# Optimization experiments

Measured on AMD Instinct MI355X. Metric: run time of the kernel, lower is better.

Reference implementation:

```python
import jax, jax.numpy as jnp
import numpy as np

T_MAX = 0.3  # clamp ceiling for effective opacity (t_max init kwarg)


def setup_inputs() -> dict:
    key = jax.random.key(0)
    k0, k1, k2 = jax.random.split(key, 3)
    B, n_blobs, d_s, d_f = 1024, 131072, 64, 256
    return {
        "query": jax.random.normal(k0, (B, d_s), dtype=jnp.float32),
        "mu": jax.random.normal(k1, (n_blobs, d_s), dtype=jnp.float32) * 0.02,
        "log_var": jnp.zeros((n_blobs, d_s), dtype=jnp.float32),
        "raw_alpha": jnp.zeros((n_blobs,), dtype=jnp.float32),
        "features": jax.random.normal(k2, (n_blobs, d_f), dtype=jnp.float32) * 0.02,
        "log_tau": jnp.asarray(np.log(128.0), dtype=jnp.float32),
        "k": 16,
    }


def reference(query, mu, log_var, raw_alpha, features, log_tau, k):
    # query: [B, d_s]; mu/log_var: [N, d_s]; features: [N, d_f]
    tau = jnp.exp(log_tau)
    inv_var = jnp.exp(-log_var)                              # [N, d_s]
    # Mahalanobis distance expanded to avoid the [B, N, d_s] diff tensor:
    # sum_d (q - mu)^2 * iv = q^2.iv - 2 q.(mu*iv) + sum(mu^2*iv)
    q2 = jnp.einsum('bd,nd->bn', query * query, inv_var)      # [B, N]
    cross = jnp.einsum('bd,nd->bn', query, mu * inv_var)      # [B, N]
    m2 = jnp.sum(mu * mu * inv_var, axis=-1)                  # [N]
    mahal = q2 - 2.0 * cross + m2[None, :]
    K_all = jnp.exp(-0.5 * mahal / tau)                       # [B, N]
    alpha = jax.nn.sigmoid(raw_alpha)                         # [N]
    scores = K_all * alpha[None, :]
    top_scores, top_idx = jax.lax.top_k(scores, k)            # [B, k]

    # Gather selected blobs and recompute exact kernel (as in the original render)
    blob_feats = features[top_idx]                            # [B, k, d_f]
    blob_mu = mu[top_idx]                                     # [B, k, d_s]
    blob_iv = jnp.exp(-log_var[top_idx])                      # [B, k, d_s]
    diff = query[:, None, :] - blob_mu                        # [B, k, d_s]
    mahal_k = jnp.sum(diff * diff * blob_iv, axis=-1)         # [B, k]
    K_topk = jnp.exp(-0.5 * mahal_k / tau)
    blob_alpha = alpha[top_idx]                               # [B, k]

    # Alpha compositing in log space
    eff = jnp.minimum(blob_alpha * K_topk, T_MAX / k)         # [B, k]
    log_1m = jnp.log1p(-jnp.minimum(eff, 1.0 - 1e-6))
    log_cum = jnp.cumsum(log_1m, axis=-1)
    log_T = jnp.concatenate(
        [jnp.zeros_like(log_cum[:, :1]), log_cum[:, :-1]], axis=-1)
    weights = eff * jnp.exp(log_T)                            # [B, k]
    blob_meaning = jnp.einsum('bk,bkd->bd', weights, blob_feats)  # [B, d_f]
    t_residual = jnp.exp(log_cum[:, -1])                      # [B]
    return blob_meaning, t_residual
```

## Files before the change

kernel.cpp:

```cpp
#include <hip/hip_runtime.h>
#include <math.h>

#define BQ    1024
#define NB    131072
#define DS    64
#define DF    256
#define KSEL  16

#define QT    128
#define BC    64
#define PCH   64
#define NCHUNK (NB / BC)
#define CHUNKS_PER_BLK (NCHUNK/PCH)

#define CH_BYTES   32768
#define SPLIT_OFF  16384

typedef __bf16 bf16x8 __attribute__((ext_vector_type(8)));
typedef float  f32x4  __attribute__((ext_vector_type(4)));
typedef unsigned long long u64;

#define ENC_NEGINF 0x007FFFFFu

__device__ __forceinline__ unsigned map_f32(float s) {
    unsigned u = __float_as_uint(s);
    return (u & 0x80000000u) ? ~u : (u | 0x80000000u);
}

__device__ __forceinline__ float unmap_f32(unsigned e) {
    return __uint_as_float((e & 0x80000000u) ? (e & 0x7FFFFFFFu) : ~e);
}

__device__ __forceinline__ void async_cp16(const void* g, void* l) {
    __builtin_amdgcn_global_load_lds(
        (const __attribute__((address_space(1))) unsigned int*)g,
        (__attribute__((address_space(3))) unsigned int*)l, 16, 0, 0);
}

__global__ __launch_bounds__(256)
void prep_kernel(const float* __restrict__ mu,
                 const float* __restrict__ log_var,
                 const float* __restrict__ raw_alpha,
                 const float* __restrict__ log_tau_p,
                 char* __restrict__ bprep,
                 float* __restrict__ m2a,
                 unsigned* __restrict__ gcut)
{
    int gid  = blockIdx.x * 256 + threadIdx.x;
    if (gid < BQ) gcut[gid] = ENC_NEGINF;
    int blob = gid >> 3;
    int dd   = gid & 7;

    const float* mrow = mu      + (size_t)blob * DS + dd * 8;
    const float* vrow = log_var + (size_t)blob * DS + dd * 8;
    float4 ma = ((const float4*)mrow)[0], mb = ((const float4*)mrow)[1];
    float4 va = ((const float4*)vrow)[0], vb = ((const float4*)vrow)[1];
    float m[8] = {ma.x, ma.y, ma.z, ma.w, mb.x, mb.y, mb.z, mb.w};
    float lv[8] = {va.x, va.y, va.z, va.w, vb.x, vb.y, vb.z, vb.w};

    bf16x8 hiv, liv, hmv, lmv;
    float p = 0.0f;
    #pragma unroll
    for (int j = 0; j < 8; ++j) {
        float iv = __expf(-lv[j]);
        float mv = m[j] * iv;
        p += m[j] * mv;
        __bf16 h1 = (__bf16)iv;  hiv[j] = h1; liv[j] = (__bf16)(iv - (float)h1);
        __bf16 h2 = (__bf16)mv;  hmv[j] = h2; lmv[j] = (__bf16)(mv - (float)h2);
    }
    p += __shfl_xor(p, 1);
    p += __shfl_xor(p, 2);
    p += __shfl_xor(p, 4);

    int c  = blob >> 6;
    int nt = (blob >> 4) & 3;
    int bl = blob & 15;
    int lane  = (dd & 3) * 16 + bl;
    int ks_iv = dd >> 2;
    int ks_mv = 2 + (dd >> 2);
    size_t b_iv = (size_t)c * CH_BYTES + nt * 4096 + ks_iv * 1024 + lane * 16;
    size_t b_mv = (size_t)c * CH_BYTES + nt * 4096 + ks_mv * 1024 + lane * 16;
    *(bf16x8*)(bprep + b_iv)             = hiv;
    *(bf16x8*)(bprep + b_iv + SPLIT_OFF) = liv;
    *(bf16x8*)(bprep + b_mv)             = hmv;
    *(bf16x8*)(bprep + b_mv + SPLIT_OFF) = lmv;

    if (dd == 0) {
        float la = -log1pf(__expf(-raw_alpha[blob]));
        float inv_nhit = -2.0f * __expf(log_tau_p[0]);
        m2a[blob] = p + la * inv_nhit;
    }
}

__device__ __forceinline__ void ins16(float (&ts)[16], int (&ti)[16],
                                      float& mymin, float s, int idx)
{
    float v0[8]; int j0[8];
    #pragma unroll
    for (int i = 0; i < 8; ++i) {
        bool b = ts[2*i+1] < ts[2*i];
        v0[i] = b ? ts[2*i+1] : ts[2*i];
        j0[i] = (i << 1) | (b ? 1 : 0);
    }
    float v1[4]; int j1[4];
    #pragma unroll
    for (int i = 0; i < 4; ++i) {
        bool b = v0[2*i+1] < v0[2*i];
        v1[i] = b ? v0[2*i+1] : v0[2*i];
        j1[i] = b ? j0[2*i+1] : j0[2*i];
    }
    float v2[2]; int j2[2];
    #pragma unroll
    for (int i = 0; i < 2; ++i) {
        bool b = v1[2*i+1] < v1[2*i];
        v2[i] = b ? v1[2*i+1] : v1[2*i];
        j2[i] = b ? j1[2*i+1] : j1[2*i];
    }
    int am = (v2[1] < v2[0]) ? j2[1] : j2[0];
    #pragma unroll
    for (int i = 0; i < 16; ++i) {
        bool b = (i == am);
        ts[i] = b ? s : ts[i];
        ti[i] = b ? idx : ti[i];
    }
    float n0[8];
    #pragma unroll
    for (int i = 0; i < 8; ++i) n0[i] = fminf(ts[2*i], ts[2*i+1]);
    float n1[4];
    #pragma unroll
    for (int i = 0; i < 4; ++i) n1[i] = fminf(n0[2*i], n0[2*i+1]);
    mymin = fminf(fminf(n1[0], n1[1]), fminf(n1[2], n1[3]));
}

__device__ __forceinline__ float mux16(const f32x4 (&a)[4], int i)
{
    float v = a[0][0];
    v = (i == 1)  ? a[0][1] : v;  v = (i == 2)  ? a[0][2] : v;  v = (i == 3)  ? a[0][3] : v;
    v = (i == 4)  ? a[1][0] : v;  v = (i == 5)  ? a[1][1] : v;  v = (i == 6)  ? a[1][2] : v;
    v = (i == 7)  ? a[1][3] : v;  v = (i == 8)  ? a[2][0] : v;  v = (i == 9)  ? a[2][1] : v;
    v = (i == 10) ? a[2][2] : v;  v = (i == 11) ? a[2][3] : v;  v = (i == 12) ? a[3][0] : v;
    v = (i == 13) ? a[3][1] : v;  v = (i == 14) ? a[3][2] : v;  v = (i == 15) ? a[3][3] : v;
    return v;
}

__device__ __forceinline__ u64 shflxor64(u64 m, int mask)
{
    unsigned hi = __shfl_xor((unsigned)(m >> 32), mask);
    unsigned lo = __shfl_xor((unsigned)(m & 0xFFFFFFFFu), mask);
    return ((u64)hi << 32) | lo;
}

__global__ __launch_bounds__(256, 2)
void score_topk_kernel(const float* __restrict__ query,
                       const char* __restrict__ bprep,
                       const float* __restrict__ m2a,
                       const float* __restrict__ log_tau_p,
                       u64* __restrict__ cand,
                       unsigned* __restrict__ gcut)
{
    __shared__ __align__(16) short Bs[CH_BYTES / 2];

    const int tid   = threadIdx.x;
    const int lane  = tid & 63;
    const int quad  = lane >> 4;
    const int mrow  = lane & 15;
    const int wv    = tid >> 6;
    const int qbase = blockIdx.y * QT;

    const float nhit     = -0.5f * expf(-log_tau_p[0]);
    const float inv_nhit = 1.0f / nhit;

    bf16x8 ahi[2][4], alo[2][4];
    #pragma unroll
    for (int mt = 0; mt < 2; ++mt) {
        const float* qrow = query + (size_t)(qbase + wv * 32 + mt * 16 + mrow) * DS;
        #pragma unroll
        for (int ks = 0; ks < 4; ++ks) {
            int kq = ks * 32 + quad * 8;
            int d0 = kq & 63;
            bool lin = kq >= 64;
            bf16x8 h, l;
            #pragma unroll
            for (int j = 0; j < 8; ++j) {
                float v = qrow[d0 + j];
                float x = lin ? (-2.0f * v) : (v * v);
                __bf16 hb = (__bf16)x;
                h[j] = hb;
                l[j] = (__bf16)(x - (float)hb);
            }
            ahi[mt][ks] = h; alo[mt][ks] = l;
        }
    }

    float ts0[16], ts1[16]; int ti0[16], ti1[16];
    #pragma unroll
    for (int i = 0; i < 16; ++i) {
        ts0[i] = -INFINITY; ti0[i] = 0;
        ts1[i] = -INFINITY; ti1[i] = 0;
    }
    float my0 = -INFINITY, my1 = -INFINITY;
    unsigned* const gs0 = gcut + qbase + wv * 32 + mrow;
    unsigned* const gs1 = gcut + qbase + wv * 32 + 16 + mrow;

    const char* BsB = (const char*)Bs;

    int c = blockIdx.x;
    {
        const char* src = bprep + (size_t)c * CH_BYTES;
        #pragma unroll
        for (int i = 0; i < 8; ++i) {
            int s = tid + i * 256;
            async_cp16(src + s * 16, (void*)(BsB + s * 16));
        }
    }
    __syncthreads();

    for (int it = 0; it < CHUNKS_PER_BLK; ++it) {
        const int nbase = c * BC;
        const int cn    = c + PCH;
        const bool more = (it + 1) < CHUNKS_PER_BLK;

        float p0 = my0;
        p0 = fmaxf(p0, __shfl_xor(p0, 16)); p0 = fmaxf(p0, __shfl_xor(p0, 32));
        float p1 = my1;
        p1 = fmaxf(p1, __shfl_xor(p1, 16)); p1 = fmaxf(p1, __shfl_xor(p1, 32));
        unsigned e0 = ENC_NEGINF, e1 = ENC_NEGINF;
        if (quad == 0) e0 = atomicMax(gs0, map_f32(p0));
        if (quad == 1) e1 = atomicMax(gs1, map_f32(p1));

        f32x4 aA[4];
        #pragma unroll
        for (int nt = 0; nt < 4; ++nt)
            aA[nt] = *(const f32x4*)&m2a[(size_t)(nbase + nt * 16 + quad * 4)];

        f32x4 acc[2][4];
        #pragma unroll
        for (int nt = 0; nt < 4; ++nt) {
            bf16x8 bh[4], bl[4];
            #pragma unroll
            for (int ks = 0; ks < 4; ++ks) {
                bh[ks] = *(const bf16x8*)(BsB + nt * 4096 + ks * 1024 + lane * 16);
                bl[ks] = *(const bf16x8*)(BsB + SPLIT_OFF + nt * 4096 + ks * 1024 + lane * 16);
            }
            #pragma unroll
            for (int mt = 0; mt < 2; ++mt) {
                f32x4 a = {0.0f, 0.0f, 0.0f, 0.0f};
                #pragma unroll
                for (int ks = 0; ks < 4; ++ks) {
                    a = __builtin_amdgcn_mfma_f32_16x16x32_bf16(bh[ks], ahi[mt][ks], a, 0, 0, 0);
                    a = __builtin_amdgcn_mfma_f32_16x16x32_bf16(bl[ks], ahi[mt][ks], a, 0, 0, 0);
                    a = __builtin_amdgcn_mfma_f32_16x16x32_bf16(bh[ks], alo[mt][ks], a, 0, 0, 0);
                }
                acc[mt][nt] = a;
            }
        }
        __syncthreads();

        if (more) {
            const char* src = bprep + (size_t)cn * CH_BYTES;
            #pragma unroll
            for (int i = 0; i < 8; ++i) {
                int s = tid + i * 256;
                async_cp16(src + s * 16, (void*)(BsB + s * 16));
            }
        }

        if (it == 0) {
            #pragma unroll
            for (int nt = 0; nt < 4; ++nt)
                #pragma unroll
                for (int reg = 0; reg < 4; ++reg) {
                    int idx = nbase + nt * 16 + quad * 4 + reg;
                    float s0 = nhit * (acc[0][nt][reg] + aA[nt][reg]);
                    float s1 = nhit * (acc[1][nt][reg] + aA[nt][reg]);
                    ts0[nt * 4 + reg] = s0; ti0[nt * 4 + reg] = idx;
                    ts1[nt * 4 + reg] = s1; ti1[nt * 4 + reg] = idx;
                }
            float n0[8], n1[8];
            #pragma unroll
            for (int i = 0; i < 8; ++i) {
                n0[i] = fminf(ts0[2*i], ts0[2*i+1]);
                n1[i] = fminf(ts1[2*i], ts1[2*i+1]);
            }
            my0 = fminf(fminf(fminf(n0[0], n0[1]), fminf(n0[2], n0[3])),
                        fminf(fminf(n0[4], n0[5]), fminf(n0[6], n0[7])));
            my1 = fminf(fminf(fminf(n1[0], n1[1]), fminf(n1[2], n1[3])),
                        fminf(fminf(n1[4], n1[5]), fminf(n1[6], n1[7])));
        } else {
            unsigned ee0 = __shfl(e0, mrow);
            unsigned ee1 = __shfl(e1, 16 + mrow);
            const float gc0 = fmaxf(unmap_f32(ee0), p0);
            const float gc1 = fmaxf(unmap_f32(ee1), p1);

            {
                float cut = fmaxf(my0, gc0);
                float T = cut * inv_nhit;
                T = T + fabsf(T) * 2e-7f;
                unsigned gm = 0u;
                #pragma unroll
                for (int nt = 0; nt < 4; ++nt) {
                    float u0 = acc[0][nt][0] + aA[nt][0];
                    float u1 = acc[0][nt][1] + aA[nt][1];
                    float u2 = acc[0][nt][2] + aA[nt][2];
                    float u3 = acc[0][nt][3] + aA[nt][3];
                    acc[0][nt][0] = u0; acc[0][nt][1] = u1;
                    acc[0][nt][2] = u2; acc[0][nt][3] = u3;
                    if (u0 < T) gm |= 1u << (nt * 4);
                    if (u1 < T) gm |= 1u << (nt * 4 + 1);
                    if (u2 < T) gm |= 1u << (nt * 4 + 2);
                    if (u3 < T) gm |= 1u << (nt * 4 + 3);
                }
                while (__any(gm != 0u)) {
                    if (gm) {
                        int i = __ffs(gm) - 1; gm &= gm - 1u;
                        float s = nhit * mux16(acc[0], i);
                        if (s > cut) {
                            ins16(ts0, ti0, my0, s, nbase + (i >> 2) * 16 + quad * 4 + (i & 3));
                            cut = fmaxf(my0, gc0);
                            T = cut * inv_nhit;
                            T = T + fabsf(T) * 2e-7f;
                        }
                    }
                }
            }
            {
                float cut = fmaxf(my1, gc1);
                float T = cut * inv_nhit;
                T = T + fabsf(T) * 2e-7f;
                unsigned gm = 0u;
                #pragma unroll
                for (int nt = 0; nt < 4; ++nt) {
                    float u0 = acc[1][nt][0] + aA[nt][0];
                    float u1 = acc[1][nt][1] + aA[nt][1];
                    float u2 = acc[1][nt][2] + aA[nt][2];
                    float u3 = acc[1][nt][3] + aA[nt][3];
                    acc[1][nt][0] = u0; acc[1][nt][1] = u1;
                    acc[1][nt][2] = u2; acc[1][nt][3] = u3;
                    if (u0 < T) gm |= 1u << (nt * 4);
                    if (u1 < T) gm |= 1u << (nt * 4 + 1);
                    if (u2 < T) gm |= 1u << (nt * 4 + 2);
                    if (u3 < T) gm |= 1u << (nt * 4 + 3);
                }
                while (__any(gm != 0u)) {
                    if (gm) {
                        int i = __ffs(gm) - 1; gm &= gm - 1u;
                        float s = nhit * mux16(acc[1], i);
                        if (s > cut) {
                            ins16(ts1, ti1, my1, s, nbase + (i >> 2) * 16 + quad * 4 + (i & 3));
                            cut = fmaxf(my1, gc1);
                            T = cut * inv_nhit;
                            T = T + fabsf(T) * 2e-7f;
                        }
                    }
                }
            }
        }

        __syncthreads();
        c = cn;
    }

    #pragma unroll
    for (int mt = 0; mt < 2; ++mt) {
        u64 k[16];
        #pragma unroll
        for (int i = 0; i < 16; ++i) {
            float  tsv = (mt == 0) ? ts0[i] : ts1[i];
            int    tiv = (mt == 0) ? ti0[i] : ti1[i];
            k[i] = ((u64)map_f32(tsv) << 32) | (u64)(0xFFFFFFFFu - (unsigned)tiv);
        }
        u64 outv[4];
        #pragma unroll
        for (int r = 0; r < 16; ++r) {
            u64 m = k[0];
            #pragma unroll
            for (int j = 1; j < 16; ++j) if (k[j] > m) m = k[j];
            u64 o = shflxor64(m, 16); if (o > m) m = o;
            o = shflxor64(m, 32);     if (o > m) m = o;
            #pragma unroll
            for (int j = 0; j < 16; ++j) if (k[j] == m) k[j] = 0ull;
            if ((r & 3) == quad) outv[r >> 2] = m;
        }
        u64* dst = cand + ((size_t)blockIdx.x * BQ + qbase + wv * 32 + mt * 16 + mrow) * KSEL;
        #pragma unroll
        for (int j = 0; j < 4; ++j)
            dst[quad + 4 * j] = outv[j];
    }
}

__global__ __launch_bounds__(256)
void merge_composite_kernel(const float* __restrict__ query,
                            const float* __restrict__ mu,
                            const float* __restrict__ log_var,
                            const float* __restrict__ raw_alpha,
                            const float* __restrict__ features,
                            const float* __restrict__ log_tau_p,
                            const u64* __restrict__ cand,
                            float* __restrict__ out)
{
    const int q   = blockIdx.x;
    const int tid = threadIdx.x;
    const int wv = tid >> 6, lane = tid & 63;

    __shared__ u64   wtop[4 * KSEL];
    __shared__ int   sel[KSEL];
    __shared__ float w_sh[KSEL];
    __shared__ float mah[KSEL];
    __shared__ float alp[KSEL];

    u64 k[4];
    #pragma unroll
    for (int r = 0; r < 4; ++r) {
        int g = wv * 256 + r * 64 + lane;
        k[r] = cand[((size_t)(g >> 4) * BQ + q) * KSEL + (g & 15)];
    }

    for (int r = 0; r < KSEL; ++r) {
        u64 m = k[0];
        #pragma unroll
        for (int j = 1; j < 4; ++j) if (k[j] > m) m = k[j];
        #pragma unroll
        for (int off = 32; off > 0; off >>= 1) {
            unsigned hi = __shfl_xor((unsigned)(m >> 32), off);
            unsigned lo = __shfl_xor((unsigned)(m & 0xFFFFFFFFu), off);
            u64 o = ((u64)hi << 32) | lo;
            if (o > m) m = o;
        }
        if (lane == 0) wtop[wv * KSEL + r] = m;
        #pragma unroll
        for (int j = 0; j < 4; ++j) if (k[j] == m) k[j] = 0ull;
    }
    __syncthreads();

    if (wv == 0) {
        u64 kk = wtop[lane];
        for (int r = 0; r < KSEL; ++r) {
            u64 m = kk;
            #pragma unroll
            for (int off = 32; off > 0; off >>= 1) {
                unsigned hi = __shfl_xor((unsigned)(m >> 32), off);
                unsigned lo = __shfl_xor((unsigned)(m & 0xFFFFFFFFu), off);
                u64 o = ((u64)hi << 32) | lo;
                if (o > m) m = o;
            }
            if (kk == m) kk = 0ull;
            if (lane == 0)
                sel[r] = (int)(0xFFFFFFFFu - (unsigned)(m & 0xFFFFFFFFull));
        }
    }
    __syncthreads();

    for (int r = wv; r < KSEL; r += 4) {
        int bi = sel[r];
        float qd = query[(size_t)q * DS + lane];
        float mv = mu[(size_t)bi * DS + lane];
        float d  = qd - mv;
        float t  = d * d * expf(-log_var[(size_t)bi * DS + lane]);
        #pragma unroll
        for (int off = 32; off > 0; off >>= 1) t += __shfl_down(t, off);
        if (lane == 0) {
            mah[r] = t;
            alp[r] = 1.0f / (1.0f + expf(-raw_alpha[bi]));
        }
    }
    __syncthreads();

    if (tid == 0) {
        float tau = expf(log_tau_p[0]);
        float cap = 0.3f / 16.0f;
        float logT = 0.0f;
        for (int r = 0; r < KSEL; ++r) {
            float K   = expf(-0.5f * mah[r] / tau);
            float eff = fminf(alp[r] * K, cap);
            w_sh[r]   = eff * expf(logT);
            logT     += log1pf(-fminf(eff, 1.0f - 1e-6f));
        }
        out[(size_t)BQ * DF + q] = expf(logT);
    }
    __syncthreads();

    {
        float a = 0.0f;
        #pragma unroll
        for (int r = 0; r < KSEL; ++r)
            a += w_sh[r] * features[(size_t)sel[r] * DF + tid];
        out[(size_t)q * DF + tid] = a;
    }
}

extern "C" void kernel_launch(void* const* d_in, const int* in_sizes, int n_in,
                              void* d_out, int out_size, void* d_ws, size_t ws_size,
                              hipStream_t stream)
{
    (void)in_sizes; (void)n_in; (void)out_size; (void)ws_size;
    const float* query     = (const float*)d_in[0];
    const float* mu        = (const float*)d_in[1];
    const float* log_var   = (const float*)d_in[2];
    const float* raw_alpha = (const float*)d_in[3];
    const float* features  = (const float*)d_in[4];
    const float* log_tau   = (const float*)d_in[5];
    float* out = (float*)d_out;

    char*  bprep = (char*)d_ws;
    float* m2a   = (float*)((char*)d_ws + (size_t)NCHUNK * CH_BYTES);
    u64*   cand  = (u64*)((char*)d_ws + (size_t)NCHUNK * CH_BYTES + (size_t)NB * 2 * 4);
    unsigned* gcut = (unsigned*)(out + (size_t)BQ * DF);

    prep_kernel<<<(NB * 8) / 256, 256, 0, stream>>>(mu, log_var, raw_alpha, log_tau,
                                                    bprep, m2a, gcut);

    dim3 g2(PCH, BQ / QT);
    score_topk_kernel<<<g2, 256, 0, stream>>>(query, bprep, m2a, log_tau, cand, gcut);

    merge_composite_kernel<<<BQ, 256, 0, stream>>>(query, mu, log_var, raw_alpha,
                                                   features, log_tau, cand, out);
}
```

Before: 557.7 us.

## Process two chunks per iteration to halve barriers and atomic cut syncs

The main loop now loads two 32KB chunks per iteration into a doubled 64KB shared buffer. It computes both MFMA score tiles back to back, then screens both against the same global cutoff. This halves the number of __syncthreads, atomicMax cutoff exchanges and loop iterations, and gives the MFMA pipe longer uninterrupted work. The m2a loads move after the MFMAs. The cost is twice the LDS per block, which with launch_bounds(256,2) may limit occupancy, more accumulator registers, and a cutoff that is refreshed less often, so screening may let through more candidates.

```diff
diff --git a/kernel.cpp b/kernel.cpp
--- a/kernel.cpp
+++ b/kernel.cpp
@@ -11,7 +11,8 @@
 #define BC    64
 #define PCH   64
 #define NCHUNK (NB / BC)
-#define CHUNKS_PER_BLK (NCHUNK/PCH)
+#define NPAIR  16
+#define CPQ   (PCH * KSEL)
 
 #define CH_BYTES   32768
 #define SPLIT_OFF  16384
@@ -150,6 +151,42 @@
     return ((u64)hi << 32) | lo;
 }
 
+__device__ __forceinline__ void screen_half(
+    f32x4 (&acc)[4], const f32x4 (&aA)[4], int nbase, int quad,
+    float gc, float nhit, float inv_nhit,
+    float (&ts)[16], int (&ti)[16], float& my)
+{
+    float cut = fmaxf(my, gc);
+    float T = cut * inv_nhit;
+    T = T + fabsf(T) * 2e-7f;
+    unsigned gm = 0u;
+    #pragma unroll
+    for (int nt = 0; nt < 4; ++nt) {
+        float u0 = acc[nt][0] + aA[nt][0];
+        float u1 = acc[nt][1] + aA[nt][1];
+        float u2 = acc[nt][2] + aA[nt][2];
+        float u3 = acc[nt][3] + aA[nt][3];
+        acc[nt][0] = u0; acc[nt][1] = u1;
+        acc[nt][2] = u2; acc[nt][3] = u3;
+        if (u0 < T) gm |= 1u << (nt * 4);
+        if (u1 < T) gm |= 1u << (nt * 4 + 1);
+        if (u2 < T) gm |= 1u << (nt * 4 + 2);
+        if (u3 < T) gm |= 1u << (nt * 4 + 3);
+    }
+    while (__any(gm != 0u)) {
+        if (gm) {
+            int i = __ffs(gm) - 1; gm &= gm - 1u;
+            float s = nhit * mux16(acc, i);
+            if (s > cut) {
+                ins16(ts, ti, my, s, nbase + (i >> 2) * 16 + quad * 4 + (i & 3));
+                cut = fmaxf(my, gc);
+                T = cut * inv_nhit;
+                T = T + fabsf(T) * 2e-7f;
+            }
+        }
+    }
+}
+
 __global__ __launch_bounds__(256, 2)
 void score_topk_kernel(const float* __restrict__ query,
                        const char* __restrict__ bprep,
@@ -158,7 +195,7 @@
                        u64* __restrict__ cand,
                        unsigned* __restrict__ gcut)
 {
-    __shared__ __align__(16) short Bs[CH_BYTES / 2];
+    __shared__ __align__(16) short Bs[CH_BYTES];
 
     const int tid   = threadIdx.x;
     const int lane  = tid & 63;
@@ -206,19 +243,23 @@
 
     int c = blockIdx.x;
     {
-        const char* src = bprep + (size_t)c * CH_BYTES;
+        const char* srcA = bprep + (size_t)c * CH_BYTES;
+        const char* srcB = bprep + (size_t)(c + PCH) * CH_BYTES;
+        char* dst = (char*)Bs;
         #pragma unroll
         for (int i = 0; i < 8; ++i) {
             int s = tid + i * 256;
-            async_cp16(src + s * 16, (void*)(BsB + s * 16));
+            async_cp16(srcA + s * 16, dst + s * 16);
+            async_cp16(srcB + s * 16, dst + CH_BYTES + s * 16);
         }
     }
     __syncthreads();
 
-    for (int it = 0; it < CHUNKS_PER_BLK; ++it) {
-        const int nbase = c * BC;
-        const int cn    = c + PCH;
-        const bool more = (it + 1) < CHUNKS_PER_BLK;
+    for (int it = 0; it < NPAIR; ++it) {
+        const int nbaseA = c * BC;
+        const int nbaseB = (c + PCH) * BC;
+        const int cn     = c + 2 * PCH;
+        const bool more  = (it + 1) < NPAIR;
 
         float p0 = my0;
         p0 = fmaxf(p0, __shfl_xor(p0, 16)); p0 = fmaxf(p0, __shfl_xor(p0, 32));
@@ -228,12 +269,7 @@
         if (quad == 0) e0 = atomicMax(gs0, map_f32(p0));
         if (quad == 1) e1 = atomicMax(gs1, map_f32(p1));
 
-        f32x4 aA[4];
-        #pragma unroll
-        for (int nt = 0; nt < 4; ++nt)
-            aA[nt] = *(const f32x4*)&m2a[(size_t)(nbase + nt * 16 + quad * 4)];
-
-        f32x4 acc[2][4];
+        f32x4 accA[2][4], accB[2][4];
         #pragma unroll
         for (int nt = 0; nt < 4; ++nt) {
             bf16x8 bh[4], bl[4];
@@ -251,28 +287,63 @@
                     a = __builtin_amdgcn_mfma_f32_16x16x32_bf16(bl[ks], ahi[mt][ks], a, 0, 0, 0);
                     a = __builtin_amdgcn_mfma_f32_16x16x32_bf16(bh[ks], alo[mt][ks], a, 0, 0, 0);
                 }
-                acc[mt][nt] = a;
+                accA[mt][nt] = a;
+            }
+        }
+        #pragma unroll
+        for (int nt = 0; nt < 4; ++nt) {
+            bf16x8 bh[4], bl[4];
+            #pragma unroll
+            for (int ks = 0; ks < 4; ++ks) {
+                bh[ks] = *(const bf16x8*)(BsB + CH_BYTES + nt * 4096 + ks * 1024 + lane * 16);
+                bl[ks] = *(const bf16x8*)(BsB + CH_BYTES + SPLIT_OFF + nt * 4096 + ks * 1024 + lane * 16);
+            }
+            #pragma unroll
+            for (int mt = 0; mt < 2; ++mt) {
+                f32x4 a = {0.0f, 0.0f, 0.0f, 0.0f};
+                #pragma unroll
+                for (int ks = 0; ks < 4; ++ks) {
+                    a = __builtin_amdgcn_mfma_f32_16x16x32_bf16(bh[ks], ahi[mt][ks], a, 0, 0, 0);
+                    a = __builtin_amdgcn_mfma_f32_16x16x32_bf16(bl[ks], ahi[mt][ks], a, 0, 0, 0);
+                    a = __builtin_amdgcn_mfma_f32_16x16x32_bf16(bh[ks], alo[mt][ks], a, 0, 0, 0);
+                }
+                accB[mt][nt] = a;
             }
         }
         __syncthreads();
 
         if (more) {
-            const char* src = bprep + (size_t)cn * CH_BYTES;
+            const char* srcA = bprep + (size_t)cn * CH_BYTES;
+            const char* srcB = bprep + (size_t)(cn + PCH) * CH_BYTES;
+            char* dst = (char*)Bs;
             #pragma unroll
             for (int i = 0; i < 8; ++i) {
                 int s = tid + i * 256;
-                async_cp16(src + s * 16, (void*)(BsB + s * 16));
-            }
-        }
+                async_cp16(srcA + s * 16, dst + s * 16);
+                async_cp16(srcB + s * 16, dst + CH_BYTES + s * 16);
+            }
+        }
+
+        f32x4 aAa[4], aAb[4];
+        #pragma unroll
+        for (int nt = 0; nt < 4; ++nt) {
+            aAa[nt] = *(const f32x4*)&m2a[(size_t)(nbaseA + nt * 16 + quad * 4)];
+            aAb[nt] = *(const f32x4*)&m2a[(size_t)(nbaseB + nt * 16 + quad * 4)];
+        }
+
+        unsigned ee0 = __shfl(e0, mrow);
+        unsigned ee1 = __shfl(e1, 16 + mrow);
+        const float gc0 = fmaxf(unmap_f32(ee0), p0);
+        const float gc1 = fmaxf(unmap_f32(ee1), p1);
 
         if (it == 0) {
             #pragma unroll
             for (int nt = 0; nt < 4; ++nt)
                 #pragma unroll
                 for (int reg = 0; reg < 4; ++reg) {
-                    int idx = nbase + nt * 16 + quad * 4 + reg;
-                    float s0 = nhit * (acc[0][nt][reg] + aA[nt][reg]);
-                    float s1 = nhit * (acc[1][nt][reg] + aA[nt][reg]);
+                    int idx = nbaseA + nt * 16 + quad * 4 + reg;
+                    float s0 = nhit * (accA[0][nt][reg] + aAa[nt][reg]);
+                    float s1 = nhit * (accA[1][nt][reg] + aAa[nt][reg]);
                     ts0[nt * 4 + reg] = s0; ti0[nt * 4 + reg] = idx;
                     ts1[nt * 4 + reg] = s1; ti1[nt * 4 + reg] = idx;
                 }
@@ -287,74 +358,11 @@
             my1 = fminf(fminf(fminf(n1[0], n1[1]), fminf(n1[2], n1[3])),
                         fminf(fminf(n1[4], n1[5]), fminf(n1[6], n1[7])));
         } else {
-            unsigned ee0 = __shfl(e0, mrow);
-            unsigned ee1 = __shfl(e1, 16 + mrow);
-            const float gc0 = fmaxf(unmap_f32(ee0), p0);
-            const float gc1 = fmaxf(unmap_f32(ee1), p1);
-
-            {
-                float cut = fmaxf(my0, gc0);
-                float T = cut * inv_nhit;
-                T = T + fabsf(T) * 2e-7f;
-                unsigned gm = 0u;
-                #pragma unroll
-                for (int nt = 0; nt < 4; ++nt) {
-                    float u0 = acc[0][nt][0] + aA[nt][0];
-                    float u1 = acc[0][nt][1] + aA[nt][1];
-                    float u2 = acc[0][nt][2] + aA[nt][2];
-                    float u3 = acc[0][nt][3] + aA[nt][3];
-                    acc[0][nt][0] = u0; acc[0][nt][1] = u1;
-                    acc[0][nt][2] = u2; acc[0][nt][3] = u3;
-                    if (u0 < T) gm |= 1u << (nt * 4);
-                    if (u1 < T) gm |= 1u << (nt * 4 + 1);
-                    if (u2 < T) gm |= 1u << (nt * 4 + 2);
-                    if (u3 < T) gm |= 1u << (nt * 4 + 3);
-                }
-                while (__any(gm != 0u)) {
-                    if (gm) {
-                        int i = __ffs(gm) - 1; gm &= gm - 1u;
-                        float s = nhit * mux16(acc[0], i);
-                        if (s > cut) {
-                            ins16(ts0, ti0, my0, s, nbase + (i >> 2) * 16 + quad * 4 + (i & 3));
-                            cut = fmaxf(my0, gc0);
-                            T = cut * inv_nhit;
-                            T = T + fabsf(T) * 2e-7f;
-                        }
-                    }
-                }
-            }
-            {
-                float cut = fmaxf(my1, gc1);
-                float T = cut * inv_nhit;
-                T = T + fabsf(T) * 2e-7f;
-                unsigned gm = 0u;
-                #pragma unroll
-                for (int nt = 0; nt < 4; ++nt) {
-                    float u0 = acc[1][nt][0] + aA[nt][0];
-                    float u1 = acc[1][nt][1] + aA[nt][1];
-                    float u2 = acc[1][nt][2] + aA[nt][2];
-                    float u3 = acc[1][nt][3] + aA[nt][3];
-                    acc[1][nt][0] = u0; acc[1][nt][1] = u1;
-                    acc[1][nt][2] = u2; acc[1][nt][3] = u3;
-                    if (u0 < T) gm |= 1u << (nt * 4);
-                    if (u1 < T) gm |= 1u << (nt * 4 + 1);
-                    if (u2 < T) gm |= 1u << (nt * 4 + 2);
-                    if (u3 < T) gm |= 1u << (nt * 4 + 3);
-                }
-                while (__any(gm != 0u)) {
-                    if (gm) {
-                        int i = __ffs(gm) - 1; gm &= gm - 1u;
-                        float s = nhit * mux16(acc[1], i);
-                        if (s > cut) {
-                            ins16(ts1, ti1, my1, s, nbase + (i >> 2) * 16 + quad * 4 + (i & 3));
-                            cut = fmaxf(my1, gc1);
-                            T = cut * inv_nhit;
-                            T = T + fabsf(T) * 2e-7f;
-                        }
-                    }
-                }
-            }
-        }
+            screen_half(accA[0], aAa, nbaseA, quad, gc0, nhit, inv_nhit, ts0, ti0, my0);
+            screen_half(accA[1], aAa, nbaseA, quad, gc1, nhit, inv_nhit, ts1, ti1, my1);
+        }
+        screen_half(accB[0], aAb, nbaseB, quad, gc0, nhit, inv_nhit, ts0, ti0, my0);
+        screen_half(accB[1], aAb, nbaseB, quad, gc1, nhit, inv_nhit, ts1, ti1, my1);
 
         __syncthreads();
         c = cn;
```

After: 624.4 us. 1.12x slower.
